# Performance work log

Measured on AMD Instinct MI355X. Metric: run time of the kernel, lower is better.

Reference implementation:

```python
import jax, jax.numpy as jnp
import numpy as np
from jax import lax

B, N_SITES, FEAT, BOND, OUT = 2048, 128, 64, 32, 256
CORE_SCALE = 0.02  # keeps the 128-step matrix product finite


def setup_inputs() -> dict:
    key = jax.random.key(0)
    ks = jax.random.split(key, 6)
    return {
        "x": jax.random.normal(ks[0], (B, N_SITES, FEAT), dtype=jnp.float32),
        "cores": jax.random.normal(ks[1], (N_SITES, BOND, FEAT, BOND), dtype=jnp.float32) * CORE_SCALE,
        "start": jax.random.normal(ks[2], (1, BOND), dtype=jnp.float32),
        "end": jax.random.normal(ks[3], (BOND, 1), dtype=jnp.float32),
        "fc_w": jax.random.normal(ks[4], (OUT, 1), dtype=jnp.float32),
        "fc_b": jax.random.normal(ks[5], (OUT,), dtype=jnp.float32),
    }


def reference(x, cores, start, end, fc_w, fc_b):
    # x: [B, N, F]; cores: [N, D, F, D]; start: [1, D]; end: [D, 1]
    b = x.shape[0]
    res0 = jnp.broadcast_to(start, (b, start.shape[1]))  # [B, D]

    def step(res, site):
        xi, core = site  # xi: [B, F], core: [D, F, D]
        m = jnp.einsum('bf,dfr->bdr', xi, core)  # per-site transfer matrix [B, D, D]
        return jnp.einsum('bd,bdr->br', res, m), None

    res, _ = lax.scan(step, res0, (jnp.swapaxes(x, 0, 1), cores))
    val = res @ end  # [B, 1]
    return val @ fc_w.T + fc_b  # [B, OUT]
```

## Files before the change

### kernel.cpp

```cpp
#include <hip/hip_runtime.h>


#define NSITES 128
#define FEATD  64
#define BOND   32
#define OUTD   256
#define BT     16
#define SEGLEN 16
#define NSEG   (NSITES / SEGLEN)
#define NBT    (2048 / BT)

#define RSTRIDE 48
#define BSTRIDE 1552

typedef __attribute__((ext_vector_type(4))) float float4v;

__device__ __forceinline__ unsigned pk4_fp8(float a, float b, float c, float d) {
    int v = __builtin_amdgcn_cvt_pk_fp8_f32(a, b, 0, false);
    v = __builtin_amdgcn_cvt_pk_fp8_f32(c, d, v, true);
    return (unsigned)v;
}

__global__ __launch_bounds__(256)
void prep_cores8(const float* __restrict__ cores, unsigned char* __restrict__ core8) {
    __shared__ float tile[FEATD][BOND + 4];
    const int nd = blockIdx.x;
    const int t  = threadIdx.x;
    const float* src = cores + (size_t)nd * (FEATD * BOND);
    {
        int base = t * 8;
        int f = base >> 5, r0 = base & 31;
        float4 v0 = *(const float4*)(src + base);
        float4 v1 = *(const float4*)(src + base + 4);
        tile[f][r0 + 0] = v0.x; tile[f][r0 + 1] = v0.y;
        tile[f][r0 + 2] = v0.z; tile[f][r0 + 3] = v0.w;
        tile[f][r0 + 4] = v1.x; tile[f][r0 + 5] = v1.y;
        tile[f][r0 + 6] = v1.z; tile[f][r0 + 7] = v1.w;
    }
    __syncthreads();
    const int r = t >> 3, f0 = (t & 7) * 8;
    const float s = 16.0f;
    unsigned lo = pk4_fp8(tile[f0 + 0][r] * s, tile[f0 + 1][r] * s,
                          tile[f0 + 2][r] * s, tile[f0 + 3][r] * s);
    unsigned hi = pk4_fp8(tile[f0 + 4][r] * s, tile[f0 + 5][r] * s,
                          tile[f0 + 6][r] * s, tile[f0 + 7][r] * s);
    uint2 w; w.x = lo; w.y = hi;
    *(uint2*)(core8 + ((size_t)nd * BOND + r) * FEATD + f0) = w;
}

__global__ __launch_bounds__(512, 4)
void mps_seg(const float* __restrict__ x, const unsigned char* __restrict__ core8,
             unsigned char* __restrict__ Pout) {
    __shared__ __align__(16) unsigned char MS[BT * BSTRIDE];
    __shared__ __align__(16) unsigned char PS[BT * BSTRIDE];
    __shared__ __align__(16) unsigned char XS[BT * 72];

    const int t    = threadIdx.x;
    const int wave = t >> 6;
    const int lane = t & 63;
    const int cl   = lane & 15;
    const int q    = lane >> 4;
    const int bt   = blockIdx.x;
    const int seg  = blockIdx.y;
    const int b0   = bt * BT;

    {
        int b = t >> 5, d = t & 31;
        unsigned w[8];
#pragma unroll
        for (int dw = 0; dw < 8; ++dw)
            w[dw] = ((d >> 2) == dw) ? (0x58u << ((d & 3) * 8)) : 0u;
        uint4* p = (uint4*)&PS[b * BSTRIDE + d * RSTRIDE];
        p[0] = make_uint4(w[0], w[1], w[2], w[3]);
        p[1] = make_uint4(w[4], w[5], w[6], w[7]);
    }

    const int xb = t >> 5, xf = (t & 31) * 2;
    float2 xf2 = *(const float2*)(x + ((size_t)(b0 + xb) * NSITES + seg * SEGLEN) * FEATD + xf);

    for (int k = 0; k < SEGLEN; ++k) {
        const int n = seg * SEGLEN + k;

        long af[16];
        {
            const unsigned char* base = core8 + (size_t)n * (1024 * FEATD);
#pragma unroll
            for (int i = 0; i < 8; ++i) {
                const unsigned char* p =
                    base + (size_t)((wave * 8 + i) * 16 + cl) * FEATD + q * 8;
                af[i * 2 + 0] = *(const long*)p;
                af[i * 2 + 1] = *(const long*)(p + 32);
            }
        }

        {
            int v = __builtin_amdgcn_cvt_pk_fp8_f32(xf2.x, xf2.y, 0, false);
            *(unsigned short*)&XS[xb * 72 + xf] = (unsigned short)(v & 0xffff);
        }
        __syncthreads();

        long bx0 = *(const long*)&XS[cl * 72 + q * 8];
        long bx1 = *(const long*)&XS[cl * 72 + 32 + q * 8];
        float4v acc[8];
#pragma unroll
        for (int i = 0; i < 8; ++i) {
            float4v z = {0.f, 0.f, 0.f, 0.f};
            z = __builtin_amdgcn_mfma_f32_16x16x32_fp8_fp8(af[i * 2 + 0], bx0, z, 0, 0, 0);
            acc[i] = __builtin_amdgcn_mfma_f32_16x16x32_fp8_fp8(af[i * 2 + 1], bx1, z, 0, 0, 0);
        }

#pragma unroll
        for (int p = 0; p < 2; ++p)
#pragma unroll
            for (int g = 0; g < 4; ++g) {
                unsigned w = pk4_fp8(acc[0 + p][g], acc[2 + p][g],
                                     acc[4 + p][g], acc[6 + p][g]);
                *(unsigned*)&MS[cl * BSTRIDE + (16 * p + 4 * q + g) * RSTRIDE + wave * 4] = w;
            }

        if (k + 1 < SEGLEN)
            xf2 = *(const float2*)(x + ((size_t)(b0 + xb) * NSITES + n + 1) * FEATD + xf);

        __syncthreads();

        long pa[2][2], pb[2][2];
#pragma unroll
        for (int bi = 0; bi < 2; ++bi) {
            int bb = wave * 2 + bi;
#pragma unroll
            for (int h = 0; h < 2; ++h) {
                pa[bi][h] = *(const long*)&MS[bb * BSTRIDE + (h * 16 + cl) * RSTRIDE + q * 8];
                pb[bi][h] = *(const long*)&PS[bb * BSTRIDE + (h * 16 + cl) * RSTRIDE + q * 8];
            }
        }
        float4v pacc[2][2][2];
#pragma unroll
        for (int bi = 0; bi < 2; ++bi)
#pragma unroll
            for (int I = 0; I < 2; ++I)
#pragma unroll
                for (int J = 0; J < 2; ++J) {
                    float4v z = {0.f, 0.f, 0.f, 0.f};
                    pacc[bi][I][J] =
                        __builtin_amdgcn_mfma_f32_16x16x32_fp8_fp8(pa[bi][I], pb[bi][J], z, 0, 0, 0);
                }
#pragma unroll
        for (int bi = 0; bi < 2; ++bi) {
            int bb = wave * 2 + bi;
#pragma unroll
            for (int I = 0; I < 2; ++I)
#pragma unroll
                for (int J = 0; J < 2; ++J) {
                    float4v c = pacc[bi][I][J];
                    unsigned w = pk4_fp8(c[0] * 0.0625f, c[1] * 0.0625f,
                                         c[2] * 0.0625f, c[3] * 0.0625f);
                    *(unsigned*)&PS[bb * BSTRIDE + (J * 16 + cl) * RSTRIDE + I * 16 + q * 4] = w;
                }
        }
    }

    __syncthreads();
    {
        int b = t >> 5, d = t & 31;
        const uint4* p = (const uint4*)&PS[b * BSTRIDE + d * RSTRIDE];
        uint4* g = (uint4*)(Pout + (((size_t)seg * 2048 + b0 + b) * 1024 + d * 32));
        g[0] = p[0];
        g[1] = p[1];
    }
}

__global__ __launch_bounds__(256)
void combine(const unsigned char* __restrict__ Pout, const float* __restrict__ startv,
             const float* __restrict__ endv, const float* __restrict__ fc_w,
             const float* __restrict__ fc_b, float* __restrict__ out) {
    __shared__ __align__(16) unsigned char st[8 * 1024];
    __shared__ float resA[8][33], resB[8][33];
    __shared__ float val[8];
    const int t  = threadIdx.x;
    const int b0 = blockIdx.x * 8;
    const int bb = t >> 5, r = t & 31;

    resA[bb][r] = startv[r];
    for (int s = 0; s < NSEG; ++s) {
        {
            const uint4* g = (const uint4*)(Pout + ((size_t)s * 2048 + b0) * 1024 + (size_t)t * 32);
            uint4* p = (uint4*)&st[t * 32];
            p[0] = g[0];
            p[1] = g[1];
        }
        __syncthreads();
        const float* rin = (s & 1) ? &resB[bb][0] : &resA[bb][0];
        float* rout      = (s & 1) ? &resA[bb][0] : &resB[bb][0];
        float acc = 0.f;
#pragma unroll
        for (int d = 0; d < BOND; ++d) {
            int byte = st[bb * 1024 + d * 32 + r];
            acc += rin[d] * __builtin_amdgcn_cvt_f32_fp8(byte, 0);
        }
        rout[r] = acc * 0.0625f;
        __syncthreads();
    }
    float prod = resA[bb][r] * endv[r];
#pragma unroll
    for (int off = 16; off >= 1; off >>= 1) prod += __shfl_down(prod, off, 32);
    if (r == 0) val[bb] = prod;
    __syncthreads();

    const float v = val[t >> 5];
    const int j0 = (t & 31) * 8;
    const int ob = b0 + (t >> 5);
#pragma unroll
    for (int i = 0; i < 2; ++i) {
        int j = j0 + i * 4;
        float4 w4 = *(const float4*)(fc_w + j);
        float4 bbv = *(const float4*)(fc_b + j);
        float4 o;
        o.x = v * w4.x + bbv.x;
        o.y = v * w4.y + bbv.y;
        o.z = v * w4.z + bbv.z;
        o.w = v * w4.w + bbv.w;
        *(float4*)(out + (size_t)ob * OUTD + j) = o;
    }
}

extern "C" void kernel_launch(void* const* d_in, const int* in_sizes, int n_in,
                              void* d_out, int out_size, void* d_ws, size_t ws_size,
                              hipStream_t stream) {
    const float* x      = (const float*)d_in[0];
    const float* cores  = (const float*)d_in[1];
    const float* startv = (const float*)d_in[2];
    const float* endv   = (const float*)d_in[3];
    const float* fc_w   = (const float*)d_in[4];
    const float* fc_b   = (const float*)d_in[5];
    float* out = (float*)d_out;

    unsigned char* core8 = (unsigned char*)d_ws;
    unsigned char* Pout  = core8 + (size_t)NSITES * 1024 * FEATD;

    prep_cores8<<<NSITES * BOND, 256, 0, stream>>>(cores, core8);
    mps_seg<<<dim3(NBT, NSEG), 512, 0, stream>>>(x, core8, Pout);
    combine<<<2048 / 8, 256, 0, stream>>>(Pout, startv, endv, fc_w, fc_b, out);
}
```

Measured before the change: 244.5 us.

## Replace segmented matrix-product scan with sequential vector contraction kernel

The old version split the chain into segments, multiplied the 32x32 transfer matrices together with MFMA, and combined segment products in a separate kernel. The new kernel carries only the bond vector through all 128 sites. It builds each site's transfer matrix with fp8 MFMA, stores it as fp16 in double-buffered LDS, and folds it into the vector with fdot2. Core and x loads are software-pipelined one site ahead, and the final readout is fused into the same kernel. This removes the matrix-matrix work and the intermediate global buffer, but parallelism drops to 128 blocks that each run a 128-step serial chain.

New measurement: 495.3 us. 2.03x slower.

```diff
diff --git a/kernel.cpp b/kernel.cpp
--- a/kernel.cpp
+++ b/kernel.cpp
@@ -6,19 +6,90 @@
 #define BOND   32
 #define OUTD   256
 #define BT     16
-#define SEGLEN 16
-#define NSEG   (NSITES / SEGLEN)
-#define NBT    (2048 / BT)
-
-#define RSTRIDE 48
-#define BSTRIDE 1552
+#define NBLK   (2048 / BT)
+
+#define MBAT   2064
+#define MBUF   (BT * MBAT)
+#define RESOFF (2 * MBUF)
+#define RESBAT 80
+#define VALOFF (RESOFF + BT * RESBAT)
+#define LDSSZ  (VALOFF + 64)
 
 typedef __attribute__((ext_vector_type(4))) float float4v;
-
+typedef __fp16 h2 __attribute__((ext_vector_type(2)));
+
+union h2u { h2 h; unsigned u; };
+
+__device__ __forceinline__ unsigned pkrtz(float a, float b) {
+    h2u v; v.h = __builtin_amdgcn_cvt_pkrtz(a, b); return v.u;
+}
+__device__ __forceinline__ float dot2(unsigned a, unsigned b, float acc) {
+    h2u x, y; x.u = a; y.u = b;
+    return __builtin_amdgcn_fdot2(x.h, y.h, acc, false);
+}
 __device__ __forceinline__ unsigned pk4_fp8(float a, float b, float c, float d) {
     int v = __builtin_amdgcn_cvt_pk_fp8_f32(a, b, 0, false);
     v = __builtin_amdgcn_cvt_pk_fp8_f32(c, d, v, true);
     return (unsigned)v;
+}
+__device__ __forceinline__ long mk64(unsigned lo, unsigned hi) {
+    return (long)(((unsigned long long)hi << 32) | lo);
+}
+
+__device__ __forceinline__ void xcvt2(const float* xl, int n, long& o0, long& o1) {
+    const float* p = xl + (size_t)n * FEATD;
+    float4 a = *(const float4*)p,        b = *(const float4*)(p + 4);
+    float4 c = *(const float4*)(p + 32), d = *(const float4*)(p + 36);
+    o0 = mk64(pk4_fp8(a.x, a.y, a.z, a.w), pk4_fp8(b.x, b.y, b.z, b.w));
+    o1 = mk64(pk4_fp8(c.x, c.y, c.z, c.w), pk4_fp8(d.x, d.y, d.z, d.w));
+}
+
+#define AF_LOAD(A, s_) { const unsigned char* p_ = cb + (size_t)(s_) * 65536; \
+    _Pragma("unroll") for (int i_ = 0; i_ < 8; ++i_) { \
+        (A)[2*i_+0] = *(const long*)(p_ + i_*1024); \
+        (A)[2*i_+1] = *(const long*)(p_ + i_*1024 + 32); } }
+
+__device__ __forceinline__ void build_pack(const long af[16], long bx0, long bx1,
+                                           unsigned char* Mw, int wbase,
+                                           int qb0, int qb1) {
+    float4v acc[8];
+#pragma unroll
+    for (int i = 0; i < 8; ++i) {
+        float4v z = {0.f, 0.f, 0.f, 0.f};
+        z = __builtin_amdgcn_mfma_f32_16x16x32_fp8_fp8(af[2*i+0], bx0, z, 0, 0, 0);
+        acc[i] = __builtin_amdgcn_mfma_f32_16x16x32_fp8_fp8(af[2*i+1], bx1, z, 0, 0, 0);
+    }
+    const float s = 0.0625f;
+#pragma unroll
+    for (int i = 0; i < 8; ++i) {
+        unsigned d0 = pkrtz(acc[i][0] * s, acc[i][1] * s);
+        unsigned d1 = pkrtz(acc[i][2] * s, acc[i][3] * s);
+        int addr = wbase + (i >> 1) * 64 + (((i & 1) ^ ((i >> 2) & 1)) << 5)
+                 + (((i >> 1) & 1) ? qb1 : qb0);
+        *(unsigned long long*)&Mw[addr] = ((unsigned long long)d1 << 32) | d0;
+    }
+}
+
+__device__ __forceinline__ float fold_site(const unsigned char* L, const int aM[4],
+                                           int moff, int aR) {
+    uint4 m0 = *(const uint4*)(L + aM[0] + moff);
+    uint4 m1 = *(const uint4*)(L + aM[1] + moff);
+    uint4 m2 = *(const uint4*)(L + aM[2] + moff);
+    uint4 m3 = *(const uint4*)(L + aM[3] + moff);
+    uint4 r0 = *(const uint4*)(L + aR);
+    uint4 r1 = *(const uint4*)(L + aR + 16);
+    uint4 r2 = *(const uint4*)(L + aR + 32);
+    uint4 r3 = *(const uint4*)(L + aR + 48);
+    float a = 0.f, b = 0.f;
+    a = dot2(r0.x, m0.x, a); b = dot2(r0.y, m0.y, b);
+    a = dot2(r0.z, m0.z, a); b = dot2(r0.w, m0.w, b);
+    a = dot2(r1.x, m1.x, a); b = dot2(r1.y, m1.y, b);
+    a = dot2(r1.z, m1.z, a); b = dot2(r1.w, m1.w, b);
+    a = dot2(r2.x, m2.x, a); b = dot2(r2.y, m2.y, b);
+    a = dot2(r2.z, m2.z, a); b = dot2(r2.w, m2.w, b);
+    a = dot2(r3.x, m3.x, a); b = dot2(r3.y, m3.y, b);
+    a = dot2(r3.z, m3.z, a); b = dot2(r3.w, m3.w, b);
+    return a + b;
 }
 
 __global__ __launch_bounds__(256)
@@ -38,188 +109,102 @@
         tile[f][r0 + 6] = v1.z; tile[f][r0 + 7] = v1.w;
     }
     __syncthreads();
-    const int r = t >> 3, f0 = (t & 7) * 8;
+    const int rr = t >> 3, f0 = (t & 7) * 8;
     const float s = 16.0f;
-    unsigned lo = pk4_fp8(tile[f0 + 0][r] * s, tile[f0 + 1][r] * s,
-                          tile[f0 + 2][r] * s, tile[f0 + 3][r] * s);
-    unsigned hi = pk4_fp8(tile[f0 + 4][r] * s, tile[f0 + 5][r] * s,
-                          tile[f0 + 6][r] * s, tile[f0 + 7][r] * s);
+    unsigned lo = pk4_fp8(tile[f0 + 0][rr] * s, tile[f0 + 1][rr] * s,
+                          tile[f0 + 2][rr] * s, tile[f0 + 3][rr] * s);
+    unsigned hi = pk4_fp8(tile[f0 + 4][rr] * s, tile[f0 + 5][rr] * s,
+                          tile[f0 + 6][rr] * s, tile[f0 + 7][rr] * s);
     uint2 w; w.x = lo; w.y = hi;
-    *(uint2*)(core8 + ((size_t)nd * BOND + r) * FEATD + f0) = w;
-}
-
-__global__ __launch_bounds__(512, 4)
-void mps_seg(const float* __restrict__ x, const unsigned char* __restrict__ core8,
-             unsigned char* __restrict__ Pout) {
-    __shared__ __align__(16) unsigned char MS[BT * BSTRIDE];
-    __shared__ __align__(16) unsigned char PS[BT * BSTRIDE];
-    __shared__ __align__(16) unsigned char XS[BT * 72];
-
-    const int t    = threadIdx.x;
-    const int wave = t >> 6;
-    const int lane = t & 63;
-    const int cl   = lane & 15;
-    const int q    = lane >> 4;
-    const int bt   = blockIdx.x;
-    const int seg  = blockIdx.y;
-    const int b0   = bt * BT;
-
-    {
-        int b = t >> 5, d = t & 31;
-        unsigned w[8];
-#pragma unroll
-        for (int dw = 0; dw < 8; ++dw)
-            w[dw] = ((d >> 2) == dw) ? (0x58u << ((d & 3) * 8)) : 0u;
-        uint4* p = (uint4*)&PS[b * BSTRIDE + d * RSTRIDE];
-        p[0] = make_uint4(w[0], w[1], w[2], w[3]);
-        p[1] = make_uint4(w[4], w[5], w[6], w[7]);
-    }
-
-    const int xb = t >> 5, xf = (t & 31) * 2;
-    float2 xf2 = *(const float2*)(x + ((size_t)(b0 + xb) * NSITES + seg * SEGLEN) * FEATD + xf);
-
-    for (int k = 0; k < SEGLEN; ++k) {
-        const int n = seg * SEGLEN + k;
-
-        long af[16];
+    *(uint2*)(core8 + (((size_t)(nd >> 5) * 1024) + (size_t)rr * 32 + (nd & 31)) * 64 + f0) = w;
+}
+
+__global__ __launch_bounds__(512, 2)
+void mps_vec(const float* __restrict__ x, const unsigned char* __restrict__ core8,
+             const float* __restrict__ startv, const float* __restrict__ endv,
+             const float* __restrict__ fc_w, const float* __restrict__ fc_b,
+             float* __restrict__ out) {
+    __shared__ __align__(16) unsigned char L[LDSSZ];
+    const int t = threadIdx.x, wave = t >> 6, lane = t & 63;
+    const int cl = lane & 15, q = lane >> 4;
+    const int h = lane >> 5, r = lane & 31;
+    const int b0 = blockIdx.x * BT;
+    const int myb = wave * 2 + h;
+
+    if (t < 256) {
+        int bb = t >> 4, j = t & 15;
+        *(unsigned*)&L[RESOFF + bb * RESBAT + j * 4] = pkrtz(startv[2*j], startv[2*j+1]);
+    }
+
+    const int wbase = cl * MBAT + wave * 256 + (q & 1) * 8;
+    const int qb0 = (q >> 1) << 4, qb1 = ((q >> 1) ^ 1) << 4;
+
+    int aM[4];
+#pragma unroll
+    for (int c = 0; c < 4; ++c)
+        aM[c] = myb * MBAT + r * 64 + ((c ^ (r & 3)) << 4);
+    const int aR  = RESOFF + myb * RESBAT;
+    const int aRW = aR + (r >> 1) * 4;
+
+    const float ev = endv[r];
+
+    const unsigned char* cb = core8 + (size_t)(wave * 8192 + cl * 64 + q * 8);
+    const float* xl = x + (size_t)(b0 + cl) * NSITES * FEATD + q * 8;
+
+    long afA[16], afB[16];
+    long xA0, xA1, xB0, xB1;
+
+    AF_LOAD(afA, 0); xcvt2(xl, 0, xA0, xA1);
+    build_pack(afA, xA0, xA1, &L[0], wbase, qb0, qb1);
+    AF_LOAD(afB, 1); xcvt2(xl, 1, xB0, xB1);
+    __syncthreads();
+
+    float rn = 0.f;
+    for (int j = 0; j < NSITES / 2; ++j) {
+        const int n = 2 * j;
         {
-            const unsigned char* base = core8 + (size_t)n * (1024 * FEATD);
-#pragma unroll
-            for (int i = 0; i < 8; ++i) {
-                const unsigned char* p =
-                    base + (size_t)((wave * 8 + i) * 16 + cl) * FEATD + q * 8;
-                af[i * 2 + 0] = *(const long*)p;
-                af[i * 2 + 1] = *(const long*)(p + 32);
+            build_pack(afB, xB0, xB1, &L[MBUF], wbase, qb0, qb1);
+            const int np = (n + 2 < NSITES) ? n + 2 : NSITES - 1;
+            AF_LOAD(afA, np); xcvt2(xl, np, xA0, xA1);
+            rn = fold_site(L, aM, 0, aR);
+            float pt = __shfl_xor(rn, 1);
+            if (!(r & 1)) *(unsigned*)&L[aRW] = pkrtz(rn, pt);
+            __syncthreads();
+        }
+        {
+            if (j < NSITES / 2 - 1) {
+                build_pack(afA, xA0, xA1, &L[0], wbase, qb0, qb1);
+                const int np = (n + 3 < NSITES) ? n + 3 : NSITES - 1;
+                AF_LOAD(afB, np); xcvt2(xl, np, xB0, xB1);
             }
+            rn = fold_site(L, aM, MBUF, aR);
+            float pt = __shfl_xor(rn, 1);
+            if (!(r & 1)) *(unsigned*)&L[aRW] = pkrtz(rn, pt);
+            __syncthreads();
         }
-
-        {
-            int v = __builtin_amdgcn_cvt_pk_fp8_f32(xf2.x, xf2.y, 0, false);
-            *(unsigned short*)&XS[xb * 72 + xf] = (unsigned short)(v & 0xffff);
-        }
-        __syncthreads();
-
-        long bx0 = *(const long*)&XS[cl * 72 + q * 8];
-        long bx1 = *(const long*)&XS[cl * 72 + 32 + q * 8];
-        float4v acc[8];
-#pragma unroll
-        for (int i = 0; i < 8; ++i) {
-            float4v z = {0.f, 0.f, 0.f, 0.f};
-            z = __builtin_amdgcn_mfma_f32_16x16x32_fp8_fp8(af[i * 2 + 0], bx0, z, 0, 0, 0);
-            acc[i] = __builtin_amdgcn_mfma_f32_16x16x32_fp8_fp8(af[i * 2 + 1], bx1, z, 0, 0, 0);
-        }
-
-#pragma unroll
-        for (int p = 0; p < 2; ++p)
-#pragma unroll
-            for (int g = 0; g < 4; ++g) {
-                unsigned w = pk4_fp8(acc[0 + p][g], acc[2 + p][g],
-                                     acc[4 + p][g], acc[6 + p][g]);
-                *(unsigned*)&MS[cl * BSTRIDE + (16 * p + 4 * q + g) * RSTRIDE + wave * 4] = w;
-            }
-
-        if (k + 1 < SEGLEN)
-            xf2 = *(const float2*)(x + ((size_t)(b0 + xb) * NSITES + n + 1) * FEATD + xf);
-
-        __syncthreads();
-
-        long pa[2][2], pb[2][2];
-#pragma unroll
-        for (int bi = 0; bi < 2; ++bi) {
-            int bb = wave * 2 + bi;
-#pragma unroll
-            for (int h = 0; h < 2; ++h) {
-                pa[bi][h] = *(const long*)&MS[bb * BSTRIDE + (h * 16 + cl) * RSTRIDE + q * 8];
-                pb[bi][h] = *(const long*)&PS[bb * BSTRIDE + (h * 16 + cl) * RSTRIDE + q * 8];
-            }
-        }
-        float4v pacc[2][2][2];
-#pragma unroll
-        for (int bi = 0; bi < 2; ++bi)
-#pragma unroll
-            for (int I = 0; I < 2; ++I)
-#pragma unroll
-                for (int J = 0; J < 2; ++J) {
-                    float4v z = {0.f, 0.f, 0.f, 0.f};
-                    pacc[bi][I][J] =
-                        __builtin_amdgcn_mfma_f32_16x16x32_fp8_fp8(pa[bi][I], pb[bi][J], z, 0, 0, 0);
-                }
-#pragma unroll
-        for (int bi = 0; bi < 2; ++bi) {
-            int bb = wave * 2 + bi;
-#pragma unroll
-            for (int I = 0; I < 2; ++I)
-#pragma unroll
-                for (int J = 0; J < 2; ++J) {
-                    float4v c = pacc[bi][I][J];
-                    unsigned w = pk4_fp8(c[0] * 0.0625f, c[1] * 0.0625f,
-                                         c[2] * 0.0625f, c[3] * 0.0625f);
-                    *(unsigned*)&PS[bb * BSTRIDE + (J * 16 + cl) * RSTRIDE + I * 16 + q * 4] = w;
-                }
-        }
-    }
-
+    }
+
+    float prod = rn * ev;
+#pragma unroll
+    for (int off = 16; off >= 1; off >>= 1) prod += __shfl_down(prod, off, 32);
+    if (r == 0) *(float*)&L[VALOFF + myb * 4] = prod;
     __syncthreads();
     {
-        int b = t >> 5, d = t & 31;
-        const uint4* p = (const uint4*)&PS[b * BSTRIDE + d * RSTRIDE];
-        uint4* g = (uint4*)(Pout + (((size_t)seg * 2048 + b0 + b) * 1024 + d * 32));
-        g[0] = p[0];
-        g[1] = p[1];
-    }
-}
-
-__global__ __launch_bounds__(256)
-void combine(const unsigned char* __restrict__ Pout, const float* __restrict__ startv,
-             const float* __restrict__ endv, const float* __restrict__ fc_w,
-             const float* __restrict__ fc_b, float* __restrict__ out) {
-    __shared__ __align__(16) unsigned char st[8 * 1024];
-    __shared__ float resA[8][33], resB[8][33];
-    __shared__ float val[8];
-    const int t  = threadIdx.x;
-    const int b0 = blockIdx.x * 8;
-    const int bb = t >> 5, r = t & 31;
-
-    resA[bb][r] = startv[r];
-    for (int s = 0; s < NSEG; ++s) {
-        {
-            const uint4* g = (const uint4*)(Pout + ((size_t)s * 2048 + b0) * 1024 + (size_t)t * 32);
-            uint4* p = (uint4*)&st[t * 32];
-            p[0] = g[0];
-            p[1] = g[1];
+        const float v = *(const float*)&L[VALOFF + (t >> 5) * 4];
+        const int j0 = (t & 31) * 8;
+        const int ob = b0 + (t >> 5);
+#pragma unroll
+        for (int i = 0; i < 2; ++i) {
+            int jj = j0 + i * 4;
+            float4 w4  = *(const float4*)(fc_w + jj);
+            float4 bbv = *(const float4*)(fc_b + jj);
+            float4 o;
+            o.x = v * w4.x + bbv.x;
+            o.y = v * w4.y + bbv.y;
+            o.z = v * w4.z + bbv.z;
+            o.w = v * w4.w + bbv.w;
+            *(float4*)(out + (size_t)ob * OUTD + jj) = o;
         }
-        __syncthreads();
-        const float* rin = (s & 1) ? &resB[bb][0] : &resA[bb][0];
-        float* rout      = (s & 1) ? &resA[bb][0] : &resB[bb][0];
-        float acc = 0.f;
-#pragma unroll
-        for (int d = 0; d < BOND; ++d) {
-            int byte = st[bb * 1024 + d * 32 + r];
-            acc += rin[d] * __builtin_amdgcn_cvt_f32_fp8(byte, 0);
-        }
-        rout[r] = acc * 0.0625f;
-        __syncthreads();
-    }
-    float prod = resA[bb][r] * endv[r];
-#pragma unroll
-    for (int off = 16; off >= 1; off >>= 1) prod += __shfl_down(prod, off, 32);
-    if (r == 0) val[bb] = prod;
-    __syncthreads();
-
-    const float v = val[t >> 5];
-    const int j0 = (t & 31) * 8;
-    const int ob = b0 + (t >> 5);
-#pragma unroll
-    for (int i = 0; i < 2; ++i) {
-        int j = j0 + i * 4;
-        float4 w4 = *(const float4*)(fc_w + j);
-        float4 bbv = *(const float4*)(fc_b + j);
-        float4 o;
-        o.x = v * w4.x + bbv.x;
-        o.y = v * w4.y + bbv.y;
-        o.z = v * w4.z + bbv.z;
-        o.w = v * w4.w + bbv.w;
-        *(float4*)(out + (size_t)ob * OUTD + j) = o;
     }
 }
 
@@ -235,9 +220,7 @@
     float* out = (float*)d_out;
 
     unsigned char* core8 = (unsigned char*)d_ws;
-    unsigned char* Pout  = core8 + (size_t)NSITES * 1024 * FEATD;
 
     prep_cores8<<<NSITES * BOND, 256, 0, stream>>>(cores, core8);
-    mps_seg<<<dim3(NBT, NSEG), 512, 0, stream>>>(x, core8, Pout);
-    combine<<<2048 / 8, 256, 0, stream>>>(Pout, startv, endv, fc_w, fc_b, out);
-}
+    mps_vec<<<NBLK, 512, 0, stream>>>(x, core8, startv, endv, fc_w, fc_b, out);
+}
```
